# Performance work log

Measured on AMD Instinct MI355X. Metric: run time of the kernel, lower is better.

Reference implementation:

```python
import jax, jax.numpy as jnp
import numpy as np

HEADS = 4
DIM_HEAD = 64


def setup_inputs() -> dict:
    key = jax.random.key(0)
    k1, k2, k3, k4 = jax.random.split(key, 4)
    dim = 256
    hidden = HEADS * DIM_HEAD  # 256
    x = jax.random.normal(k1, (16, dim, 64, 64), dtype=jnp.float32)
    # 1x1 conv weights stored as [out_c, in_c]
    w_qkv = jax.random.normal(k2, (3 * hidden, dim), dtype=jnp.float32) * (1.0 / np.sqrt(dim))
    w_out = jax.random.normal(k3, (dim, hidden), dtype=jnp.float32) * (1.0 / np.sqrt(hidden))
    b_out = jax.random.normal(k4, (dim,), dtype=jnp.float32) * 0.01
    gamma = jnp.ones((dim,), dtype=jnp.float32) * 1e-05
    return {"x": x, "w_qkv": w_qkv, "w_out": w_out, "b_out": b_out, "gamma": gamma}


def reference(x, w_qkv, w_out, b_out, gamma):
    b, c, h, w = x.shape
    n = h * w
    # 1x1 conv == channel matmul
    qkv = jnp.einsum('oc,bchw->bohw', w_qkv, x)  # [b, 3*heads*dh, h, w]
    qkv = qkv.reshape(b, 3, HEADS, DIM_HEAD, n)  # channel split order: (qkv, heads, c)
    q, k, v = qkv[:, 0], qkv[:, 1], qkv[:, 2]    # each [b, heads, dh, n]
    k = jax.nn.softmax(k, axis=-1)               # softmax over spatial tokens
    context = jnp.einsum('bhdn,bhen->bhde', k, v)  # [b, heads, dh, dh]
    out = jnp.einsum('bhde,bhdn->bhen', context, q)  # [b, heads, dh, n]
    out = out.reshape(b, HEADS * DIM_HEAD, h, w)
    y = jnp.einsum('oc,bchw->bohw', w_out, out) + b_out[None, :, None, None]
    return y * gamma[None, :, None, None] + x
```

## Files before the change

kernel.cpp:

```cpp
#include <hip/hip_runtime.h>
#include <stdint.h>

typedef short s16x8 __attribute__((ext_vector_type(8)));
typedef float f32x4 __attribute__((ext_vector_type(4)));

__device__ __forceinline__ float bits2f(unsigned short u) {
    union { unsigned int i; float f; } c; c.i = ((unsigned int)u) << 16; return c.f;
}
__device__ __forceinline__ unsigned short f2bits(float f) {
    union { float f; unsigned int i; } c; c.f = f;
    unsigned int x = c.i;
    unsigned int r = (x + 0x7FFFu + ((x >> 16) & 1u)) >> 16;
    return (unsigned short)r;
}
__device__ __forceinline__ unsigned int pack2(float a, float b) {
    return (unsigned int)f2bits(a) | ((unsigned int)f2bits(b) << 16);
}

__global__ __launch_bounds__(256) void k_cvt(
    const float* __restrict__ src, unsigned short* __restrict__ dst, int n8)
{
    int i = blockIdx.x * 256 + threadIdx.x;
    if (i >= n8) return;
    const float* s = src + (size_t)i * 8;
    float4 a = *(const float4*)s, b = *(const float4*)(s + 4);
    unsigned int q[4] = { pack2(a.x, a.y), pack2(a.z, a.w), pack2(b.x, b.y), pack2(b.z, b.w) };
    *(s16x8*)(dst + (size_t)i * 8) = *(s16x8*)q;
}

__global__ __launch_bounds__(256) void k_transpose(
    const unsigned short* __restrict__ src, unsigned short* __restrict__ dst,
    int RS, int DS)
{
    int dr = blockIdx.x * 256 + threadIdx.x;
    int c0 = blockIdx.y * 8;
    __align__(16) unsigned short tmp[8];
#pragma unroll
    for (int j = 0; j < 8; ++j) tmp[j] = src[(size_t)(c0 + j) * RS + dr];
    *(s16x8*)(dst + (size_t)dr * DS + c0) = *(s16x8*)tmp;
}

__global__ __launch_bounds__(256) void k_prepw(
    const float* __restrict__ wqkv, const float* __restrict__ wout,
    unsigned short* __restrict__ wb, unsigned short* __restrict__ wob,
    unsigned short* __restrict__ WqT)
{
    int i = blockIdx.x * 256 + threadIdx.x;
    if (i < 32768) {
        const float* s; unsigned short* d; int j;
        if (i < 24576) { s = wqkv; d = wb; j = i; }
        else           { s = wout; d = wob; j = i - 24576; }
        const float* sp = s + (size_t)j * 8;
        float4 a = *(const float4*)sp, b = *(const float4*)(sp + 4);
        unsigned int q[4] = { pack2(a.x, a.y), pack2(a.z, a.w), pack2(b.x, b.y), pack2(b.z, b.w) };
        *(s16x8*)(d + (size_t)j * 8) = *(s16x8*)q;
    } else {
        int j = i - 32768;
        int dr = j & 255, c0 = (j >> 8) * 8;
        __align__(16) unsigned short tmp[8];
#pragma unroll
        for (int jj = 0; jj < 8; ++jj)
            tmp[jj] = f2bits(wqkv[(size_t)(c0 + jj) * 256 + dr]);
        *(s16x8*)(WqT + (size_t)dr * 256 + c0) = *(s16x8*)tmp;
    }
}

__global__ __launch_bounds__(256) void k_prep(
    const float* __restrict__ x, unsigned short* __restrict__ xT)
{
    __shared__ unsigned short Ts[64][264];
    int b = blockIdx.y, n0 = blockIdx.x * 64, t = threadIdx.x;
    const float* xb = x + (size_t)b * 1048576;
#pragma unroll
    for (int i = 0; i < 16; ++i) {
        int idx = t + i * 256;
        int c = idx >> 4, nq = idx & 15;
        float4 v = *(const float4*)(xb + (size_t)c * 4096 + n0 + nq * 4);
        float vv[4] = { v.x, v.y, v.z, v.w };
#pragma unroll
        for (int e = 0; e < 4; ++e) {
            int ee = (e + c) & 3;
            Ts[nq * 4 + ee][c] = f2bits(vv[ee]);
        }
    }
    __syncthreads();
    unsigned short* xTb = xT + (size_t)b * 1048576 + (size_t)n0 * 256;
#pragma unroll
    for (int i = 0; i < 8; ++i) {
        int idx = t + i * 256;
        int nl = idx >> 5, cg = (idx & 31) * 8;
        *(s16x8*)(xTb + (size_t)nl * 256 + cg) = *(const s16x8*)&Ts[nl][cg];
    }
}

template <int BF32, int EPI>
__global__ __launch_bounds__(256) void gemm_bt(
    const unsigned short* __restrict__ A, const void* __restrict__ Bt,
    void* __restrict__ C,
    int K, int Kstep, int lda, int ldb, int ldc,
    long Abs, long Bbs, long Cbs,
    const float* __restrict__ Xres,
    const float* __restrict__ gamma,
    const float* __restrict__ bias)
{
    __shared__ unsigned short As[128][72];
    __shared__ unsigned short Bs[128][72];
    int bz = blockIdx.z;
    int b = bz & 15, kc = bz >> 4;
    int m0 = blockIdx.y * 128, n0 = blockIdx.x * 128;
    const unsigned short* Ab = A + (size_t)b * Abs + (size_t)m0 * lda + (size_t)kc * Kstep;
    size_t boff = (size_t)b * Bbs + (size_t)n0 * ldb + (size_t)kc * Kstep;
    int t = threadIdx.x;
    int w = t >> 6, l = t & 63, lm = l & 15, lq = l >> 4;
    int mw = (w >> 1) * 64, nw = (w & 1) * 64;

    f32x4 acc[4][4];
    f32x4 zero = {0.f, 0.f, 0.f, 0.f};
#pragma unroll
    for (int i = 0; i < 4; ++i)
#pragma unroll
        for (int j = 0; j < 4; ++j) acc[i][j] = zero;

    for (int kk = 0; kk < K; kk += 64) {
#pragma unroll
        for (int i = 0; i < 4; ++i) {
            int idx = t + i * 256;
            int r = idx >> 3, ch = idx & 7;
            *(s16x8*)&As[r][ch * 8] = *(const s16x8*)(Ab + (size_t)r * lda + kk + ch * 8);
            if (BF32) {
                const float* bp = (const float*)Bt + boff + (size_t)r * ldb + kk + ch * 8;
                float4 v0 = *(const float4*)bp, v1 = *(const float4*)(bp + 4);
                unsigned int q[4] = { pack2(v0.x, v0.y), pack2(v0.z, v0.w),
                                      pack2(v1.x, v1.y), pack2(v1.z, v1.w) };
                *(s16x8*)&Bs[r][ch * 8] = *(s16x8*)q;
            } else {
                const unsigned short* bp = (const unsigned short*)Bt + boff + (size_t)r * ldb + kk + ch * 8;
                *(s16x8*)&Bs[r][ch * 8] = *(const s16x8*)bp;
            }
        }
        __syncthreads();
#pragma unroll
        for (int ks = 0; ks < 2; ++ks) {
            s16x8 af[4], bfr[4];
#pragma unroll
            for (int mi = 0; mi < 4; ++mi) af[mi]  = *(const s16x8*)&As[mw + mi * 16 + lm][ks * 32 + lq * 8];
#pragma unroll
            for (int ni = 0; ni < 4; ++ni) bfr[ni] = *(const s16x8*)&Bs[nw + ni * 16 + lm][ks * 32 + lq * 8];
#pragma unroll
            for (int mi = 0; mi < 4; ++mi)
#pragma unroll
                for (int ni = 0; ni < 4; ++ni)
                    acc[mi][ni] = __builtin_amdgcn_mfma_f32_16x16x32_bf16(af[mi], bfr[ni], acc[mi][ni], 0, 0, 0);
        }
        __syncthreads();
    }

    if (EPI == 0) {
        unsigned short* Cb = (unsigned short*)C + (size_t)bz * Cbs;
#pragma unroll
        for (int mi = 0; mi < 4; ++mi)
#pragma unroll
            for (int r = 0; r < 4; ++r) {
                int m = m0 + mw + mi * 16 + lq * 4 + r;
#pragma unroll
                for (int ni = 0; ni < 4; ++ni) {
                    int n = n0 + nw + ni * 16 + lm;
                    Cb[(size_t)m * ldc + n] = f2bits(acc[mi][ni][r]);
                }
            }
    } else {
        float* Cb = (float*)C + (size_t)bz * Cbs;
        const float* Xb = Xres + (size_t)bz * Cbs;
#pragma unroll
        for (int mi = 0; mi < 4; ++mi)
#pragma unroll
            for (int r = 0; r < 4; ++r) {
                int m = m0 + mw + mi * 16 + lq * 4 + r;
                float g = gamma[m], bo = bias[m];
#pragma unroll
                for (int ni = 0; ni < 4; ++ni) {
                    int n = n0 + nw + ni * 16 + lm;
                    size_t idx = (size_t)m * ldc + n;
                    Cb[idx] = g * (acc[mi][ni][r] + bo) + Xb[idx];
                }
            }
    }
}

template <int EPI>
__global__ __launch_bounds__(256) void gemm_bn(
    const unsigned short* __restrict__ A, const float* __restrict__ B,
    void* __restrict__ C,
    int K, int lda, int ldb, int ldc,
    long Abs, long Bbs, long Cbs,
    const float* __restrict__ Xres,
    const float* __restrict__ gamma,
    const float* __restrict__ bias)
{
    __shared__ unsigned short As[128][72];
    __shared__ unsigned short Bs[64][130];
    int bz = blockIdx.z;
    int m0 = blockIdx.y * 128, n0 = blockIdx.x * 128;
    const unsigned short* Ab = A + (size_t)bz * Abs + (size_t)m0 * lda;
    const float* Bb = B + (size_t)bz * Bbs + n0;
    int t = threadIdx.x;
    int w = t >> 6, l = t & 63, lm = l & 15, lq = l >> 4;
    int mw = (w >> 1) * 64, nw = (w & 1) * 64;

    f32x4 acc[4][4];
    f32x4 zero = {0.f, 0.f, 0.f, 0.f};
#pragma unroll
    for (int i = 0; i < 4; ++i)
#pragma unroll
        for (int j = 0; j < 4; ++j) acc[i][j] = zero;

    for (int kk = 0; kk < K; kk += 64) {
#pragma unroll
        for (int i = 0; i < 4; ++i) {
            int idx = t + i * 256;
            int r = idx >> 3, ch = idx & 7;
            *(s16x8*)&As[r][ch * 8] = *(const s16x8*)(Ab + (size_t)r * lda + kk + ch * 8);
        }
#pragma unroll
        for (int i = 0; i < 4; ++i) {
            int idx = t + i * 256;
            int c = idx >> 4, cc = idx & 15;
            const float* bp = Bb + (size_t)(kk + c) * ldb + cc * 8;
            float4 v0 = *(const float4*)bp, v1 = *(const float4*)(bp + 4);
            unsigned int* q = (unsigned int*)&Bs[c][cc * 8];
            q[0] = pack2(v0.x, v0.y); q[1] = pack2(v0.z, v0.w);
            q[2] = pack2(v1.x, v1.y); q[3] = pack2(v1.z, v1.w);
        }
        __syncthreads();
#pragma unroll
        for (int ks = 0; ks < 2; ++ks) {
            s16x8 af[4];
#pragma unroll
            for (int mi = 0; mi < 4; ++mi) af[mi] = *(const s16x8*)&As[mw + mi * 16 + lm][ks * 32 + lq * 8];
#pragma unroll
            for (int ni = 0; ni < 4; ++ni) {
                s16x8 bfr;
#pragma unroll
                for (int j = 0; j < 8; ++j) bfr[j] = (short)Bs[ks * 32 + lq * 8 + j][nw + ni * 16 + lm];
#pragma unroll
                for (int mi = 0; mi < 4; ++mi)
                    acc[mi][ni] = __builtin_amdgcn_mfma_f32_16x16x32_bf16(af[mi], bfr, acc[mi][ni], 0, 0, 0);
            }
        }
        __syncthreads();
    }

#pragma unroll
    for (int mi = 0; mi < 4; ++mi)
#pragma unroll
        for (int r = 0; r < 4; ++r) {
            int m = m0 + mw + mi * 16 + lq * 4 + r;
            float g = 0.f, bo = 0.f;
            if (EPI == 1) { g = gamma[m]; bo = bias[m]; }
#pragma unroll
            for (int ni = 0; ni < 4; ++ni) {
                int n = n0 + nw + ni * 16 + lm;
                size_t idx = (size_t)m * ldc + n;
                float v = acc[mi][ni][r];
                if (EPI == 1) {
                    float* Cb = (float*)C + (size_t)bz * Cbs;
                    Cb[idx] = g * (v + bo) + Xres[(size_t)bz * Cbs + idx];
                } else {
                    unsigned short* Cb = (unsigned short*)C + (size_t)bz * Cbs;
                    Cb[idx] = f2bits(v);
                }
            }
        }
}

__global__ __launch_bounds__(256) void k_softmax(unsigned short* __restrict__ kbuf)
{
    unsigned short* p = kbuf + (size_t)blockIdx.x * 4096;
    int t = threadIdx.x;
    __shared__ float red[4];

    s16x8 r0 = *(const s16x8*)(p + t * 16);
    s16x8 r1 = *(const s16x8*)(p + t * 16 + 8);
    float v[16];
    float m = -1e30f;
#pragma unroll
    for (int i = 0; i < 8; ++i) { v[i] = bits2f((unsigned short)r0[i]); v[8 + i] = bits2f((unsigned short)r1[i]); }
#pragma unroll
    for (int i = 0; i < 16; ++i) m = fmaxf(m, v[i]);
#pragma unroll
    for (int off = 32; off >= 1; off >>= 1) m = fmaxf(m, __shfl_xor(m, off));
    if ((t & 63) == 0) red[t >> 6] = m;
    __syncthreads();
    m = fmaxf(fmaxf(red[0], red[1]), fmaxf(red[2], red[3]));
    __syncthreads();

    float s = 0.f;
#pragma unroll
    for (int i = 0; i < 16; ++i) { v[i] = __expf(v[i] - m); s += v[i]; }
#pragma unroll
    for (int off = 32; off >= 1; off >>= 1) s += __shfl_xor(s, off);
    if ((t & 63) == 0) red[t >> 6] = s;
    __syncthreads();
    s = red[0] + red[1] + red[2] + red[3];
    float inv = 1.0f / s;

    __align__(16) unsigned short otmp[16];
#pragma unroll
    for (int i = 0; i < 16; ++i) otmp[i] = f2bits(v[i] * inv);
    *(s16x8*)(p + t * 16) = *(s16x8*)(otmp);
    *(s16x8*)(p + t * 16 + 8) = *(s16x8*)(otmp + 8);
}

__global__ __launch_bounds__(256) void k_gred(
    const unsigned short* __restrict__ Gp, unsigned short* __restrict__ G)
{
    int gid = blockIdx.x * 256 + threadIdx.x;
    int b = gid >> 13;
    size_t i8 = (size_t)(gid & 8191) * 8;
    float s[8] = {0.f, 0.f, 0.f, 0.f, 0.f, 0.f, 0.f, 0.f};
#pragma unroll
    for (int kc = 0; kc < 8; ++kc) {
        s16x8 v = *(const s16x8*)(Gp + (size_t)(kc * 16 + b) * 65536 + i8);
#pragma unroll
        for (int j = 0; j < 8; ++j) s[j] += bits2f((unsigned short)v[j]);
    }
    __align__(16) unsigned short tmp[8];
#pragma unroll
    for (int j = 0; j < 8; ++j) tmp[j] = f2bits(s[j]);
    *(s16x8*)(G + (size_t)b * 65536 + i8) = *(s16x8*)tmp;
}

__global__ __launch_bounds__(256) void k_ctxw2(
    const unsigned short* __restrict__ G, const unsigned short* __restrict__ wb,
    const unsigned short* __restrict__ wob, unsigned short* __restrict__ W2)
{
    __shared__ unsigned short ctxs[64][72];
    int h = blockIdx.x, b = blockIdx.y;
    int t = threadIdx.x, w = t >> 6, l = t & 63, lm = l & 15, lq = l >> 4;
    const unsigned short* Gb = G + (size_t)b * 65536 + (size_t)(h * 64) * 256;
    const unsigned short* Wv = wb + 131072 + (size_t)(h * 64) * 256;
    f32x4 zero = {0.f, 0.f, 0.f, 0.f};

    f32x4 acc[4];
#pragma unroll
    for (int i = 0; i < 4; ++i) acc[i] = zero;
    for (int kk = 0; kk < 256; kk += 32) {
        s16x8 a = *(const s16x8*)(Gb + (size_t)(w * 16 + lm) * 256 + kk + lq * 8);
#pragma unroll
        for (int ni = 0; ni < 4; ++ni) {
            s16x8 bb = *(const s16x8*)(Wv + (size_t)(ni * 16 + lm) * 256 + kk + lq * 8);
            acc[ni] = __builtin_amdgcn_mfma_f32_16x16x32_bf16(a, bb, acc[ni], 0, 0, 0);
        }
    }
#pragma unroll
    for (int ni = 0; ni < 4; ++ni)
#pragma unroll
        for (int r = 0; r < 4; ++r)
            ctxs[w * 16 + lq * 4 + r][ni * 16 + lm] = f2bits(acc[ni][r]);
    __syncthreads();

    f32x4 acc2[4][4];
#pragma unroll
    for (int i = 0; i < 4; ++i)
#pragma unroll
        for (int j = 0; j < 4; ++j) acc2[i][j] = zero;
#pragma unroll
    for (int ks = 0; ks < 2; ++ks) {
        s16x8 af[4], bfr[4];
#pragma unroll
        for (int mi = 0; mi < 4; ++mi)
            af[mi] = *(const s16x8*)(wob + (size_t)(w * 64 + mi * 16 + lm) * 256 + h * 64 + ks * 32 + lq * 8);
#pragma unroll
        for (int ni = 0; ni < 4; ++ni) bfr[ni] = *(const s16x8*)&ctxs[ni * 16 + lm][ks * 32 + lq * 8];
#pragma unroll
        for (int mi = 0; mi < 4; ++mi)
#pragma unroll
            for (int ni = 0; ni < 4; ++ni)
                acc2[mi][ni] = __builtin_amdgcn_mfma_f32_16x16x32_bf16(af[mi], bfr[ni], acc2[mi][ni], 0, 0, 0);
    }
    unsigned short* W2b = W2 + (size_t)b * 65536;
#pragma unroll
    for (int mi = 0; mi < 4; ++mi)
#pragma unroll
        for (int r = 0; r < 4; ++r) {
            int o = w * 64 + mi * 16 + lq * 4 + r;
#pragma unroll
            for (int ni = 0; ni < 4; ++ni)
                W2b[(size_t)o * 256 + h * 64 + ni * 16 + lm] = f2bits(acc2[mi][ni][r]);
        }
}

extern "C" void kernel_launch(void* const* d_in, const int* in_sizes, int n_in,
                              void* d_out, int out_size, void* d_ws, size_t ws_size,
                              hipStream_t stream)
{
    (void)in_sizes; (void)n_in; (void)out_size;
    const float* x      = (const float*)d_in[0];
    const float* w_qkv  = (const float*)d_in[1];
    const float* w_out  = (const float*)d_in[2];
    const float* b_out  = (const float*)d_in[3];
    const float* gamma  = (const float*)d_in[4];

    char* ws = (char*)d_ws;
    const size_t NEED = 40501248;

    if (ws_size >= NEED) {
        unsigned short* xT  = (unsigned short*)ws;
        unsigned short* G   = (unsigned short*)(ws + 33554432);
        unsigned short* W2  = (unsigned short*)(ws + 35651584);
        unsigned short* W3  = (unsigned short*)(ws + 37748736);
        unsigned short* WqT = (unsigned short*)(ws + 39845888);
        unsigned short* wb  = (unsigned short*)(ws + 39976960);
        unsigned short* wob = (unsigned short*)(ws + 40370176);
        unsigned short* kbuf = (unsigned short*)d_out;
        unsigned short* Gp   = (unsigned short*)((char*)d_out + 33554432);

        k_prepw<<<dim3(160), 256, 0, stream>>>(w_qkv, w_out, wb, wob, WqT);

        k_prep<<<dim3(64, 16), 256, 0, stream>>>(x, xT);

        gemm_bt<0, 0><<<dim3(32, 2, 16), 256, 0, stream>>>(
            wb + 65536, xT, kbuf, 256, 0, 256, 256, 4096,
            0L, 1048576L, 1048576L, nullptr, nullptr, nullptr);

        k_softmax<<<dim3(4096), 256, 0, stream>>>(kbuf);

        gemm_bt<1, 0><<<dim3(2, 2, 128), 256, 0, stream>>>(
            kbuf, x, Gp, 512, 512, 4096, 4096, 256,
            1048576L, 1048576L, 65536L, nullptr, nullptr, nullptr);

        k_gred<<<dim3(512), 256, 0, stream>>>(Gp, G);

        k_ctxw2<<<dim3(4, 16), 256, 0, stream>>>(G, wb, wob, W2);

        gemm_bt<0, 0><<<dim3(2, 2, 16), 256, 0, stream>>>(
            W2, WqT, W3, 256, 0, 256, 256, 256,
            65536L, 0L, 65536L, nullptr, nullptr, nullptr);

        gemm_bt<0, 1><<<dim3(32, 2, 16), 256, 0, stream>>>(
            W3, xT, d_out, 256, 0, 256, 256, 4096,
            65536L, 1048576L, 1048576L, x, gamma, b_out);
    } else {
        unsigned short* kbuf = (unsigned short*)d_out;
        unsigned short* Gp  = (unsigned short*)(ws);
        unsigned short* G   = (unsigned short*)(ws + 16777216);
        unsigned short* W2  = (unsigned short*)(ws + 18874368);
        unsigned short* W3  = (unsigned short*)(ws + 20971520);
        unsigned short* WqT = (unsigned short*)(ws + 23068672);
        unsigned short* wb  = (unsigned short*)(ws + 23199744);
        unsigned short* wob = (unsigned short*)(ws + 23592960);

        k_cvt<<<dim3(96), 256, 0, stream>>>(w_qkv, wb, 24576);
        k_cvt<<<dim3(32), 256, 0, stream>>>(w_out, wob, 8192);
        k_transpose<<<dim3(1, 32, 1), 256, 0, stream>>>(wb, WqT, 256, 256);

        gemm_bn<0><<<dim3(32, 2, 16), 256, 0, stream>>>(
            wb + 65536, x, kbuf, 256, 256, 4096, 4096,
            0L, 1048576L, 1048576L, nullptr, nullptr, nullptr);

        k_softmax<<<dim3(4096), 256, 0, stream>>>(kbuf);

        gemm_bt<1, 0><<<dim3(2, 2, 128), 256, 0, stream>>>(
            kbuf, x, Gp, 512, 512, 4096, 4096, 256,
            1048576L, 1048576L, 65536L, nullptr, nullptr, nullptr);

        k_gred<<<dim3(512), 256, 0, stream>>>(Gp, G);
        k_ctxw2<<<dim3(4, 16), 256, 0, stream>>>(G, wb, wob, W2);

        gemm_bt<0, 0><<<dim3(2, 2, 16), 256, 0, stream>>>(
            W2, WqT, W3, 256, 0, 256, 256, 256,
            65536L, 0L, 65536L, nullptr, nullptr, nullptr);

        gemm_bn<1><<<dim3(32, 2, 16), 256, 0, stream>>>(
            W3, x, d_out, 256, 256, 4096, 4096,
            65536L, 1048576L, 1048576L, x, gamma, b_out);
    }
}
```

Before: 232.1 us.

## Use direct global-to-LDS loads in new GEMMs and bf16 x copy for context GEMM

Adds new GEMM kernels (128x128 and 64x64 tiles) that stage A/B tiles with global_load_lds and an XOR-swizzled LDS layout instead of register-staged copies. The prep kernel now also writes a bf16 copy of x so the k·v context GEMM reads bf16 instead of fp32. The split-K layout for the context GEMM changes from 8 chunks to 2, with a smaller reduction. Workspace buffers are reshuffled into d_out to make room, which adds aliasing risk and extra write traffic for the bf16 x copy.

New measurement: 230.0 us. Within noise of the previous version (-0.9%).

```diff
diff --git a/kernel.cpp b/kernel.cpp
--- a/kernel.cpp
+++ b/kernel.cpp
@@ -3,6 +3,10 @@
 
 typedef short s16x8 __attribute__((ext_vector_type(8)));
 typedef float f32x4 __attribute__((ext_vector_type(4)));
+typedef unsigned int u32x2 __attribute__((ext_vector_type(2)));
+
+typedef const __attribute__((address_space(1))) void glb_cv;
+typedef __attribute__((address_space(3))) void lds_v;
 
 __device__ __forceinline__ float bits2f(unsigned short u) {
     union { unsigned int i; float f; } c; c.i = ((unsigned int)u) << 16; return c.f;
@@ -15,6 +19,10 @@
 }
 __device__ __forceinline__ unsigned int pack2(float a, float b) {
     return (unsigned int)f2bits(a) | ((unsigned int)f2bits(b) << 16);
+}
+
+__device__ __forceinline__ void gl_lds16(const void* g, void* l) {
+    __builtin_amdgcn_global_load_lds((glb_cv*)g, (lds_v*)l, 16, 0, 0);
 }
 
 __global__ __launch_bounds__(256) void k_cvt(
@@ -66,16 +74,20 @@
 }
 
 __global__ __launch_bounds__(256) void k_prep(
-    const float* __restrict__ x, unsigned short* __restrict__ xT)
+    const float* __restrict__ x, unsigned short* __restrict__ xT,
+    unsigned short* __restrict__ xbf)
 {
     __shared__ unsigned short Ts[64][264];
     int b = blockIdx.y, n0 = blockIdx.x * 64, t = threadIdx.x;
     const float* xb = x + (size_t)b * 1048576;
+    unsigned short* xbfb = xbf + (size_t)b * 1048576;
 #pragma unroll
     for (int i = 0; i < 16; ++i) {
         int idx = t + i * 256;
         int c = idx >> 4, nq = idx & 15;
         float4 v = *(const float4*)(xb + (size_t)c * 4096 + n0 + nq * 4);
+        u32x2 q; q[0] = pack2(v.x, v.y); q[1] = pack2(v.z, v.w);
+        *(u32x2*)(xbfb + (size_t)c * 4096 + n0 + nq * 4) = q;
         float vv[4] = { v.x, v.y, v.z, v.w };
 #pragma unroll
         for (int e = 0; e < 4; ++e) {
@@ -91,6 +103,170 @@
         int nl = idx >> 5, cg = (idx & 31) * 8;
         *(s16x8*)(xTb + (size_t)nl * 256 + cg) = *(const s16x8*)&Ts[nl][cg];
     }
+}
+
+template <int EPI>
+__global__ __launch_bounds__(256) void gemm_bt2(
+    const unsigned short* __restrict__ A, const unsigned short* __restrict__ Bt,
+    void* __restrict__ C,
+    int K, int Kstep, int lda, int ldb, int ldc,
+    long Abs, long Bbs, long Cbs,
+    const float* __restrict__ Xres,
+    const float* __restrict__ gamma,
+    const float* __restrict__ bias)
+{
+    __shared__ __align__(16) unsigned short As[128 * 64];
+    __shared__ __align__(16) unsigned short Bs[128 * 64];
+    int bz = blockIdx.z;
+    int b = bz & 15, kc = bz >> 4;
+    int m0 = blockIdx.y * 128, n0 = blockIdx.x * 128;
+    const unsigned short* Ab = A + (size_t)b * Abs + (size_t)m0 * lda + (size_t)kc * Kstep;
+    const unsigned short* Bb = Bt + (size_t)b * Bbs + (size_t)n0 * ldb + (size_t)kc * Kstep;
+    int t = threadIdx.x;
+    int w = t >> 6, l = t & 63, lm = l & 15, lq = l >> 4;
+    int mw = (w >> 1) * 64, nw = (w & 1) * 64;
+
+    f32x4 acc[4][4];
+    f32x4 zero = {0.f, 0.f, 0.f, 0.f};
+#pragma unroll
+    for (int i = 0; i < 4; ++i)
+#pragma unroll
+        for (int j = 0; j < 4; ++j) acc[i][j] = zero;
+
+    for (int kk = 0; kk < K; kk += 64) {
+#pragma unroll
+        for (int i = 0; i < 4; ++i) {
+            int idx = t + i * 256;
+            int r = idx >> 3;
+            int sch = (idx & 7) ^ (r & 7);
+            int lbase = (i * 256 + w * 64) * 8;
+            gl_lds16(Ab + (size_t)r * lda + kk + sch * 8, &As[lbase]);
+            gl_lds16(Bb + (size_t)r * ldb + kk + sch * 8, &Bs[lbase]);
+        }
+        __syncthreads();
+#pragma unroll
+        for (int ks = 0; ks < 2; ++ks) {
+            s16x8 af[4], bfr[4];
+#pragma unroll
+            for (int mi = 0; mi < 4; ++mi) {
+                int row = mw + mi * 16 + lm;
+                af[mi] = *(const s16x8*)&As[row * 64 + (((ks * 4 + lq) ^ (row & 7)) << 3)];
+            }
+#pragma unroll
+            for (int ni = 0; ni < 4; ++ni) {
+                int row = nw + ni * 16 + lm;
+                bfr[ni] = *(const s16x8*)&Bs[row * 64 + (((ks * 4 + lq) ^ (row & 7)) << 3)];
+            }
+#pragma unroll
+            for (int mi = 0; mi < 4; ++mi)
+#pragma unroll
+                for (int ni = 0; ni < 4; ++ni)
+                    acc[mi][ni] = __builtin_amdgcn_mfma_f32_16x16x32_bf16(af[mi], bfr[ni], acc[mi][ni], 0, 0, 0);
+        }
+        __syncthreads();
+    }
+
+    if (EPI == 0) {
+        unsigned short* Cb = (unsigned short*)C + (size_t)bz * Cbs;
+#pragma unroll
+        for (int mi = 0; mi < 4; ++mi)
+#pragma unroll
+            for (int r = 0; r < 4; ++r) {
+                int m = m0 + mw + mi * 16 + lq * 4 + r;
+#pragma unroll
+                for (int ni = 0; ni < 4; ++ni) {
+                    int n = n0 + nw + ni * 16 + lm;
+                    Cb[(size_t)m * ldc + n] = f2bits(acc[mi][ni][r]);
+                }
+            }
+    } else {
+        float* Cb = (float*)C + (size_t)bz * Cbs;
+        const float* Xb = Xres + (size_t)bz * Cbs;
+#pragma unroll
+        for (int mi = 0; mi < 4; ++mi)
+#pragma unroll
+            for (int r = 0; r < 4; ++r) {
+                int m = m0 + mw + mi * 16 + lq * 4 + r;
+                float g = gamma[m], bo = bias[m];
+#pragma unroll
+                for (int ni = 0; ni < 4; ++ni) {
+                    int n = n0 + nw + ni * 16 + lm;
+                    size_t idx = (size_t)m * ldc + n;
+                    Cb[idx] = g * (acc[mi][ni][r] + bo) + Xb[idx];
+                }
+            }
+    }
+}
+
+__global__ __launch_bounds__(256) void gemm64(
+    const unsigned short* __restrict__ A, const unsigned short* __restrict__ Bt,
+    unsigned short* __restrict__ C,
+    int K, int Kstep, int lda, int ldb, int ldc,
+    long Abs, long Bbs, long Cbs)
+{
+    __shared__ __align__(16) unsigned short As[64 * 64];
+    __shared__ __align__(16) unsigned short Bs[64 * 64];
+    int bz = blockIdx.z;
+    int b = bz & 15, kc = bz >> 4;
+    int m0 = blockIdx.y * 64, n0 = blockIdx.x * 64;
+    const unsigned short* Ab = A + (size_t)b * Abs + (size_t)m0 * lda + (size_t)kc * Kstep;
+    const unsigned short* Bb = Bt + (size_t)b * Bbs + (size_t)n0 * ldb + (size_t)kc * Kstep;
+    int t = threadIdx.x;
+    int w = t >> 6, l = t & 63, lm = l & 15, lq = l >> 4;
+    int mw = (w >> 1) * 32, nw = (w & 1) * 32;
+
+    f32x4 acc[2][2];
+    f32x4 zero = {0.f, 0.f, 0.f, 0.f};
+#pragma unroll
+    for (int i = 0; i < 2; ++i)
+#pragma unroll
+        for (int j = 0; j < 2; ++j) acc[i][j] = zero;
+
+    for (int kk = 0; kk < K; kk += 64) {
+#pragma unroll
+        for (int i = 0; i < 2; ++i) {
+            int idx = t + i * 256;
+            int r = idx >> 3;
+            int sch = (idx & 7) ^ (r & 7);
+            int lbase = (i * 256 + w * 64) * 8;
+            gl_lds16(Ab + (size_t)r * lda + kk + sch * 8, &As[lbase]);
+            gl_lds16(Bb + (size_t)r * ldb + kk + sch * 8, &Bs[lbase]);
+        }
+        __syncthreads();
+#pragma unroll
+        for (int ks = 0; ks < 2; ++ks) {
+            s16x8 af[2], bfr[2];
+#pragma unroll
+            for (int mi = 0; mi < 2; ++mi) {
+                int row = mw + mi * 16 + lm;
+                af[mi] = *(const s16x8*)&As[row * 64 + (((ks * 4 + lq) ^ (row & 7)) << 3)];
+            }
+#pragma unroll
+            for (int ni = 0; ni < 2; ++ni) {
+                int row = nw + ni * 16 + lm;
+                bfr[ni] = *(const s16x8*)&Bs[row * 64 + (((ks * 4 + lq) ^ (row & 7)) << 3)];
+            }
+#pragma unroll
+            for (int mi = 0; mi < 2; ++mi)
+#pragma unroll
+                for (int ni = 0; ni < 2; ++ni)
+                    acc[mi][ni] = __builtin_amdgcn_mfma_f32_16x16x32_bf16(af[mi], bfr[ni], acc[mi][ni], 0, 0, 0);
+        }
+        __syncthreads();
+    }
+
+    unsigned short* Cb = C + (size_t)bz * Cbs;
+#pragma unroll
+    for (int mi = 0; mi < 2; ++mi)
+#pragma unroll
+        for (int r = 0; r < 4; ++r) {
+            int m = m0 + mw + mi * 16 + lq * 4 + r;
+#pragma unroll
+            for (int ni = 0; ni < 2; ++ni) {
+                int n = n0 + nw + ni * 16 + lm;
+                Cb[(size_t)m * ldc + n] = f2bits(acc[mi][ni][r]);
+            }
+        }
 }
 
 template <int BF32, int EPI>
@@ -311,6 +487,7 @@
     *(s16x8*)(p + t * 16 + 8) = *(s16x8*)(otmp + 8);
 }
 
+template <int NC>
 __global__ __launch_bounds__(256) void k_gred(
     const unsigned short* __restrict__ Gp, unsigned short* __restrict__ G)
 {
@@ -319,7 +496,7 @@
     size_t i8 = (size_t)(gid & 8191) * 8;
     float s[8] = {0.f, 0.f, 0.f, 0.f, 0.f, 0.f, 0.f, 0.f};
 #pragma unroll
-    for (int kc = 0; kc < 8; ++kc) {
+    for (int kc = 0; kc < NC; ++kc) {
         s16x8 v = *(const s16x8*)(Gp + (size_t)(kc * 16 + b) * 65536 + i8);
 #pragma unroll
         for (int j = 0; j < 8; ++j) s[j] += bits2f((unsigned short)v[j]);
@@ -406,38 +583,39 @@
 
     if (ws_size >= NEED) {
         unsigned short* xT  = (unsigned short*)ws;
-        unsigned short* G   = (unsigned short*)(ws + 33554432);
-        unsigned short* W2  = (unsigned short*)(ws + 35651584);
-        unsigned short* W3  = (unsigned short*)(ws + 37748736);
+        unsigned short* W3  = (unsigned short*)(ws + 33554432);
+        unsigned short* Gp  = (unsigned short*)(ws + 35651584);
         unsigned short* WqT = (unsigned short*)(ws + 39845888);
         unsigned short* wb  = (unsigned short*)(ws + 39976960);
         unsigned short* wob = (unsigned short*)(ws + 40370176);
         unsigned short* kbuf = (unsigned short*)d_out;
-        unsigned short* Gp   = (unsigned short*)((char*)d_out + 33554432);
+        unsigned short* xbf  = (unsigned short*)d_out + 16777216;
+        unsigned short* G    = (unsigned short*)d_out;
+        unsigned short* W2   = (unsigned short*)d_out + 1048576;
 
         k_prepw<<<dim3(160), 256, 0, stream>>>(w_qkv, w_out, wb, wob, WqT);
 
-        k_prep<<<dim3(64, 16), 256, 0, stream>>>(x, xT);
-
-        gemm_bt<0, 0><<<dim3(32, 2, 16), 256, 0, stream>>>(
+        k_prep<<<dim3(64, 16), 256, 0, stream>>>(x, xT, xbf);
+
+        gemm_bt2<0><<<dim3(32, 2, 16), 256, 0, stream>>>(
             wb + 65536, xT, kbuf, 256, 0, 256, 256, 4096,
             0L, 1048576L, 1048576L, nullptr, nullptr, nullptr);
 
         k_softmax<<<dim3(4096), 256, 0, stream>>>(kbuf);
 
-        gemm_bt<1, 0><<<dim3(2, 2, 128), 256, 0, stream>>>(
-            kbuf, x, Gp, 512, 512, 4096, 4096, 256,
-            1048576L, 1048576L, 65536L, nullptr, nullptr, nullptr);
-
-        k_gred<<<dim3(512), 256, 0, stream>>>(Gp, G);
+        gemm64<<<dim3(4, 4, 32), 256, 0, stream>>>(
+            kbuf, xbf, Gp, 2048, 2048, 4096, 4096, 256,
+            1048576L, 1048576L, 65536L);
+
+        k_gred<2><<<dim3(512), 256, 0, stream>>>(Gp, G);
 
         k_ctxw2<<<dim3(4, 16), 256, 0, stream>>>(G, wb, wob, W2);
 
-        gemm_bt<0, 0><<<dim3(2, 2, 16), 256, 0, stream>>>(
+        gemm64<<<dim3(4, 4, 16), 256, 0, stream>>>(
             W2, WqT, W3, 256, 0, 256, 256, 256,
-            65536L, 0L, 65536L, nullptr, nullptr, nullptr);
-
-        gemm_bt<0, 1><<<dim3(32, 2, 16), 256, 0, stream>>>(
+            65536L, 0L, 65536L);
+
+        gemm_bt2<1><<<dim3(32, 2, 16), 256, 0, stream>>>(
             W3, xT, d_out, 256, 0, 256, 256, 4096,
             65536L, 1048576L, 1048576L, x, gamma, b_out);
     } else {
@@ -464,7 +642,7 @@
             kbuf, x, Gp, 512, 512, 4096, 4096, 256,
             1048576L, 1048576L, 65536L, nullptr, nullptr, nullptr);
 
-        k_gred<<<dim3(512), 256, 0, stream>>>(Gp, G);
+        k_gred<8><<<dim3(512), 256, 0, stream>>>(Gp, G);
         k_ctxw2<<<dim3(4, 16), 256, 0, stream>>>(G, wb, wob, W2);
 
         gemm_bt<0, 0><<<dim3(2, 2, 16), 256, 0, stream>>>(
```
